# Performance work log

Hardware: AMD Instinct MI355X
Metric: run time of the kernel (lower is better)

The kernel has to match this reference:

```python
import jax, jax.numpy as jnp
import numpy as np

N_NODES = 50000
N_EDGES = 1600000
IN_CH = 128
HIDDEN = 64
OUT_DIM = 64
N_GRAPHS = 64


def setup_inputs() -> dict:
    key = jax.random.key(0)
    ks = jax.random.split(key, 8)
    x = jax.random.normal(ks[0], (N_NODES, IN_CH), dtype=jnp.float32)
    W1 = jax.random.normal(ks[1], (IN_CH, HIDDEN), dtype=jnp.float32) * (1.0 / np.sqrt(IN_CH))
    b1 = jnp.zeros((HIDDEN,), dtype=jnp.float32)
    W2 = jax.random.normal(ks[2], (HIDDEN, HIDDEN), dtype=jnp.float32) * (1.0 / np.sqrt(HIDDEN))
    b2 = jnp.zeros((HIDDEN,), dtype=jnp.float32)
    Wp = jax.random.normal(ks[3], (HIDDEN, OUT_DIM), dtype=jnp.float32) * (1.0 / np.sqrt(HIDDEN))
    bp = jnp.zeros((OUT_DIM,), dtype=jnp.float32)
    edge_index = jax.random.randint(ks[4], (2, N_EDGES), 0, N_NODES, dtype=jnp.int32)
    batch = jnp.sort(jax.random.randint(ks[5], (N_NODES,), 0, N_GRAPHS, dtype=jnp.int32))
    return {"x": x, "W1": W1, "b1": b1, "W2": W2, "b2": b2,
            "Wp": Wp, "bp": bp, "edge_index": edge_index, "batch": batch}


def _gcn_norm(edge_index, num_nodes):
    # add self-loops, then symmetric normalization D^{-1/2} (A+I) D^{-1/2}
    loop = jnp.arange(num_nodes, dtype=edge_index.dtype)
    src = jnp.concatenate([edge_index[0], loop])
    dst = jnp.concatenate([edge_index[1], loop])
    deg = jax.ops.segment_sum(jnp.ones_like(dst, dtype=jnp.float32), dst,
                              num_segments=num_nodes)
    dinv = jnp.where(deg > 0, jax.lax.rsqrt(deg), 0.0)
    norm = dinv[src] * dinv[dst]  # [E+N]
    return src, dst, norm


def _gcn_conv(x, W, b, src, dst, norm, num_nodes):
    h = x @ W                                  # [N, F_out] transform first (F_out small)
    msg = h[src] * norm[:, None]               # gather + scale  [E+N, F_out]
    agg = jax.ops.segment_sum(msg, dst, num_segments=num_nodes)
    return agg + b


def reference(x, W1, b1, W2, b2, Wp, bp, edge_index, batch):
    n = x.shape[0]
    src, dst, norm = _gcn_norm(edge_index, n)
    h = jax.nn.relu(_gcn_conv(x, W1, b1, src, dst, norm, n))
    # dropout: eval mode (identity)
    h = jax.nn.relu(_gcn_conv(h, W2, b2, src, dst, norm, n))
    # global mean pool over graphs in batch
    gsum = jax.ops.segment_sum(h, batch, num_segments=N_GRAPHS)
    cnt = jax.ops.segment_sum(jnp.ones((n,), dtype=h.dtype), batch,
                              num_segments=N_GRAPHS)
    g = gsum / jnp.maximum(cnt, 1.0)[:, None]
    return g @ Wp + bp
```

## Files before the change

kernel.cpp:

```cpp
#include <hip/hip_runtime.h>

#define N_NODES  50000
#define N_EDGESC 1600000
#define N_GRAPHS 64
#define NBUCK    196
#define CHUNK    2048
#define NBLK     782

static __device__ __forceinline__ unsigned short f2bf(float f) {
  unsigned u = __float_as_uint(f);
  u += 0x7FFF + ((u >> 16) & 1);
  return (unsigned short)(u >> 16);
}
static __device__ __forceinline__ float bfLo(unsigned u) {
  return __uint_as_float(u << 16);
}
static __device__ __forceinline__ float bfHi(unsigned u) {
  return __uint_as_float(u & 0xFFFF0000u);
}

static __device__ __forceinline__ int lowerb(const int* a, int n, int v) {
  int lo = 0, hi = n;
  while (lo < hi) { int m = (lo + hi) >> 1; if (a[m] < v) lo = m + 1; else hi = m; }
  return lo;
}

__global__ __launch_bounds__(256) void k_hist(const int* __restrict__ dst,
                                              int* __restrict__ bcnt,
                                              float* __restrict__ gsum, int E) {
  __shared__ int hist[NBUCK];
  int t = threadIdx.x, blk = blockIdx.x;
  if (t < NBUCK) hist[t] = 0;
  if (blk == 0) {
    for (int i = t; i < N_GRAPHS * 64; i += 256) gsum[i] = 0.f;
  }
  __syncthreads();
  int e0 = blk * CHUNK;
#pragma unroll
  for (int i = 0; i < CHUNK; i += 256) {
    int e = e0 + i + t;
    if (e < E) atomicAdd(&hist[dst[e] >> 8], 1);
  }
  __syncthreads();
  if (t < NBUCK) bcnt[(size_t)t * NBLK + blk] = hist[t];
}

__global__ __launch_bounds__(256) void k_cscan(int* __restrict__ bcnt,
                                               int* __restrict__ btot) {
  __shared__ int sm[256];
  int b = blockIdx.x, t = threadIdx.x;
  int* p = bcnt + (size_t)b * NBLK;
  int carry = 0;
  for (int tile = 0; tile < (NBLK + 255) / 256; ++tile) {
    int idx = tile * 256 + t;
    int v = (idx < NBLK) ? p[idx] : 0;
    sm[t] = v;
    __syncthreads();
    for (int o = 1; o < 256; o <<= 1) {
      int add = (t >= o) ? sm[t - o] : 0;
      __syncthreads();
      sm[t] += add;
      __syncthreads();
    }
    int incl = sm[t];
    int total = sm[255];
    if (idx < NBLK) p[idx] = incl - v + carry;
    carry += total;
    __syncthreads();
  }
  if (t == 0) btot[b] = carry;
}

__global__ __launch_bounds__(256) void k_scatter(const int* __restrict__ src,
                                                 const int* __restrict__ dst,
                                                 const int* __restrict__ bcnt,
                                                 const int* __restrict__ btot,
                                                 unsigned* __restrict__ bbuf, int E) {
  __shared__ int base[NBUCK], cur[NBUCK], sm[256];
  int t = threadIdx.x, blk = blockIdx.x;
  int v = (t < NBUCK) ? btot[t] : 0;
  sm[t] = v;
  __syncthreads();
  for (int o = 1; o < 256; o <<= 1) {
    int add = (t >= o) ? sm[t - o] : 0;
    __syncthreads();
    sm[t] += add;
    __syncthreads();
  }
  if (t < NBUCK) {
    base[t] = (sm[t] - v) + bcnt[(size_t)t * NBLK + blk];
    cur[t] = 0;
  }
  __syncthreads();
  int e0 = blk * CHUNK;
#pragma unroll
  for (int i = 0; i < CHUNK; i += 256) {
    int e = e0 + i + t;
    if (e < E) {
      int d = dst[e], b = d >> 8;
      int pos = base[b] + atomicAdd(&cur[b], 1);
      bbuf[pos] = ((unsigned)(d & 255) << 24) | (unsigned)src[e];
    }
  }
}

__global__ __launch_bounds__(512) void k_bsort(const unsigned* __restrict__ bbuf,
                                               const int* __restrict__ btot,
                                               int* __restrict__ csr,
                                               int* __restrict__ row_off,
                                               float* __restrict__ dinv) {
  __shared__ int hist[256], off[256], cur[256], sm[256];
  int b = blockIdx.x, t = threadIdx.x;
  if (t < 256) {
    int v = (t < NBUCK) ? btot[t] : 0;
    sm[t] = v;
    hist[t] = 0; cur[t] = 0;
  }
  __syncthreads();
  for (int o = 1; o < 256; o <<= 1) {
    int add = 0;
    if (t < 256 && t >= o) add = sm[t - o];
    __syncthreads();
    if (t < 256) sm[t] += add;
    __syncthreads();
  }
  int gb = (b > 0) ? sm[b - 1] : 0;
  int cnt = btot[b];
  const unsigned* bp = bbuf + gb;
  for (int i = t; i < cnt; i += 512) atomicAdd(&hist[bp[i] >> 24], 1);
  __syncthreads();
  if (t < 256) off[t] = hist[t];
  __syncthreads();
  for (int o = 1; o < 256; o <<= 1) {
    int add = 0;
    if (t < 256 && t >= o) add = off[t - o];
    __syncthreads();
    if (t < 256) off[t] += add;
    __syncthreads();
  }
  if (t < 256) {
    int excl = off[t] - hist[t];
    off[t] = excl;
    int idx = (b << 8) + t;
    if (idx <= N_NODES) row_off[idx] = gb + excl;
    if (idx < N_NODES)  dinv[idx] = rsqrtf((float)(hist[t] + 1));
  }
  __syncthreads();
  for (int i = t; i < cnt; i += 512) {
    unsigned v = bp[i];
    int ld = v >> 24;
    int pos = atomicAdd(&cur[ld], 1);
    csr[gb + off[ld] + pos] = (int)(v & 0xFFFFFFu);
  }
}

template <int K>
__global__ __launch_bounds__(256) void k_gemm(const float* __restrict__ x,
                                              const float* __restrict__ W,
                                              const float* __restrict__ dinv,
                                              unsigned short* __restrict__ out, int N) {
  constexpr int KS = 64;
  constexpr int KP = KS + 4;
  __shared__ float xs[64 * KP];
  __shared__ float Wl[KS * 64];
  const int t = threadIdx.x;
  const int lane = t & 63;
  const int w = t >> 6;
  const int n0 = blockIdx.x * 64;

  float acc[16];
#pragma unroll
  for (int j = 0; j < 16; ++j) acc[j] = 0.f;

  for (int h = 0; h < K / KS; ++h) {
#pragma unroll
    for (int i = 0; i < KS * 16 / 256; ++i) {
      int li = i * 256 + t;
      float4 v = reinterpret_cast<const float4*>(W + h * KS * 64)[li];
      *reinterpret_cast<float4*>(Wl + li * 4) = v;
    }
#pragma unroll
    for (int i = 0; i < 64 * (KS / 4) / 256; ++i) {
      int li = i * 256 + t;
      int row = li / (KS / 4), c4 = li % (KS / 4);
      int node = n0 + row;
      float4 v = make_float4(0.f, 0.f, 0.f, 0.f);
      if (node < N) v = reinterpret_cast<const float4*>(x + (size_t)node * K + h * KS)[c4];
      *reinterpret_cast<float4*>(xs + row * KP + c4 * 4) = v;
    }
    __syncthreads();

    const float* xr = xs + lane * KP;
    const float* wq = Wl + w * 16;
#pragma unroll 4
    for (int kp = 0; kp < KS / 4; ++kp) {
      float4 xv = *reinterpret_cast<const float4*>(xr + kp * 4);
#pragma unroll
      for (int q = 0; q < 4; ++q) {
        int k = kp * 4 + q;
        float xq = (q == 0) ? xv.x : (q == 1) ? xv.y : (q == 2) ? xv.z : xv.w;
        const float* wk = wq + k * 64;
        float4 w0 = *reinterpret_cast<const float4*>(wk);
        float4 w1 = *reinterpret_cast<const float4*>(wk + 4);
        float4 w2 = *reinterpret_cast<const float4*>(wk + 8);
        float4 w3 = *reinterpret_cast<const float4*>(wk + 12);
        acc[ 0] = fmaf(xq, w0.x, acc[ 0]);
        acc[ 1] = fmaf(xq, w0.y, acc[ 1]);
        acc[ 2] = fmaf(xq, w0.z, acc[ 2]);
        acc[ 3] = fmaf(xq, w0.w, acc[ 3]);
        acc[ 4] = fmaf(xq, w1.x, acc[ 4]);
        acc[ 5] = fmaf(xq, w1.y, acc[ 5]);
        acc[ 6] = fmaf(xq, w1.z, acc[ 6]);
        acc[ 7] = fmaf(xq, w1.w, acc[ 7]);
        acc[ 8] = fmaf(xq, w2.x, acc[ 8]);
        acc[ 9] = fmaf(xq, w2.y, acc[ 9]);
        acc[10] = fmaf(xq, w2.z, acc[10]);
        acc[11] = fmaf(xq, w2.w, acc[11]);
        acc[12] = fmaf(xq, w3.x, acc[12]);
        acc[13] = fmaf(xq, w3.y, acc[13]);
        acc[14] = fmaf(xq, w3.z, acc[14]);
        acc[15] = fmaf(xq, w3.w, acc[15]);
      }
    }
    __syncthreads();
  }

  int node = n0 + lane;
  if (node < N) {
    float dv = dinv[node];
    unsigned pk[8];
#pragma unroll
    for (int j = 0; j < 8; ++j) {
      unsigned lo = f2bf(acc[2 * j] * dv);
      unsigned hi = f2bf(acc[2 * j + 1] * dv);
      pk[j] = lo | (hi << 16);
    }
    unsigned* op = reinterpret_cast<unsigned*>(out + (size_t)node * 64 + w * 16);
    *reinterpret_cast<uint4*>(op)     = make_uint4(pk[0], pk[1], pk[2], pk[3]);
    *reinterpret_cast<uint4*>(op + 4) = make_uint4(pk[4], pk[5], pk[6], pk[7]);
  }
}

__global__ __launch_bounds__(256) void k_gather(const unsigned short* __restrict__ hs,
                                                const int* __restrict__ row_off,
                                                const int* __restrict__ csr,
                                                const float* __restrict__ dinv,
                                                const float* __restrict__ bias,
                                                float* __restrict__ out, int N) {
  const int lane = threadIdx.x & 63;
  const int slot = lane >> 3;
  const int pos  = lane & 7;
  int wid = blockIdx.x * 4 + (threadIdx.x >> 6);
  int stride = gridDim.x * 4;
  const uint4* hsq = reinterpret_cast<const uint4*>(hs);
  float4 bA = reinterpret_cast<const float4*>(bias)[pos * 2];
  float4 bB = reinterpret_cast<const float4*>(bias)[pos * 2 + 1];
  for (int i = wid; i < N; i += stride) {
    float a[8];
    {
      uint4 sv = hsq[(((unsigned)i) << 3) + pos];
      if (slot == 0) {
        a[0] = bfLo(sv.x); a[1] = bfHi(sv.x); a[2] = bfLo(sv.y); a[3] = bfHi(sv.y);
        a[4] = bfLo(sv.z); a[5] = bfHi(sv.z); a[6] = bfLo(sv.w); a[7] = bfHi(sv.w);
      } else {
#pragma unroll
        for (int k = 0; k < 8; ++k) a[k] = 0.f;
      }
    }
    const int s0 = row_off[i], s1 = row_off[i + 1];
    int j = s0;
    for (; j + 32 <= s1; j += 32) {
      int idx[4];
#pragma unroll
      for (int q = 0; q < 4; ++q) idx[q] = csr[j + 8 * q + slot];
      uint4 v[4];
#pragma unroll
      for (int q = 0; q < 4; ++q)
        v[q] = hsq[(((unsigned)idx[q]) << 3) + pos];
#pragma unroll
      for (int q = 0; q < 4; ++q) {
        a[0] += bfLo(v[q].x); a[1] += bfHi(v[q].x);
        a[2] += bfLo(v[q].y); a[3] += bfHi(v[q].y);
        a[4] += bfLo(v[q].z); a[5] += bfHi(v[q].z);
        a[6] += bfLo(v[q].w); a[7] += bfHi(v[q].w);
      }
    }
    if (j < s1) {
      int idx[4];
      bool ok[4];
#pragma unroll
      for (int q = 0; q < 4; ++q) {
        int e = j + 8 * q + slot;
        ok[q] = e < s1;
        idx[q] = csr[min(e, s1 - 1)];
      }
      uint4 v[4];
#pragma unroll
      for (int q = 0; q < 4; ++q)
        v[q] = hsq[(((unsigned)idx[q]) << 3) + pos];
#pragma unroll
      for (int q = 0; q < 4; ++q) {
        if (ok[q]) {
          a[0] += bfLo(v[q].x); a[1] += bfHi(v[q].x);
          a[2] += bfLo(v[q].y); a[3] += bfHi(v[q].y);
          a[4] += bfLo(v[q].z); a[5] += bfHi(v[q].z);
          a[6] += bfLo(v[q].w); a[7] += bfHi(v[q].w);
        }
      }
    }
#pragma unroll
    for (int k = 0; k < 8; ++k) {
      a[k] += __shfl_xor(a[k], 8);
      a[k] += __shfl_xor(a[k], 16);
      a[k] += __shfl_xor(a[k], 32);
    }
    if (slot == 0) {
      float dv = dinv[i];
      float4 rA, rB;
      rA.x = fmaxf(fmaf(a[0], dv, bA.x), 0.f);
      rA.y = fmaxf(fmaf(a[1], dv, bA.y), 0.f);
      rA.z = fmaxf(fmaf(a[2], dv, bA.z), 0.f);
      rA.w = fmaxf(fmaf(a[3], dv, bA.w), 0.f);
      rB.x = fmaxf(fmaf(a[4], dv, bB.x), 0.f);
      rB.y = fmaxf(fmaf(a[5], dv, bB.y), 0.f);
      rB.z = fmaxf(fmaf(a[6], dv, bB.z), 0.f);
      rB.w = fmaxf(fmaf(a[7], dv, bB.w), 0.f);
      float4* op = reinterpret_cast<float4*>(out + (((size_t)i) << 6) + pos * 8);
      op[0] = rA;
      op[1] = rB;
    }
  }
}

__global__ __launch_bounds__(256) void k_pool1(const float* __restrict__ h,
                                               const int* __restrict__ batch,
                                               float* __restrict__ gsum, int N) {
  int c = threadIdx.x & 63;
  int w = threadIdx.x >> 6;
  int r0 = blockIdx.x * 64 + w * 16;
  if (r0 >= N) return;
  int r1 = min(r0 + 16, N);
  int gprev = batch[r0];
  float acc = 0.f;
  for (int r = r0; r < r1; ++r) {
    int g = batch[r];
    if (g != gprev) { atomicAdd(&gsum[gprev * 64 + c], acc); acc = 0.f; gprev = g; }
    acc += h[(size_t)r * 64 + c];
  }
  atomicAdd(&gsum[gprev * 64 + c], acc);
}

__global__ void k_final(const float* __restrict__ gsum, const int* __restrict__ batch,
                        const float* __restrict__ Wp, const float* __restrict__ bp,
                        float* __restrict__ out, int N) {
  __shared__ int lb[5];
  int t = threadIdx.x;
  int g0 = blockIdx.x * 4;
  if (t < 5) lb[t] = lowerb(batch, N, g0 + t);
  __syncthreads();
  int idx = blockIdx.x * 256 + t;
  int g = idx >> 6, o = idx & 63, gl = g & 3;
  float cinv = 1.0f / fmaxf((float)(lb[gl + 1] - lb[gl]), 1.0f);
  float acc = 0.f;
#pragma unroll
  for (int k = 0; k < 64; ++k) acc += gsum[g * 64 + k] * Wp[k * 64 + o];
  out[idx] = fmaf(acc, cinv, bp[o]);
}

extern "C" void kernel_launch(void* const* d_in, const int* in_sizes, int n_in,
                              void* d_out, int out_size, void* d_ws, size_t ws_size,
                              hipStream_t stream) {
  const float* x    = (const float*)d_in[0];
  const float* W1   = (const float*)d_in[1];
  const float* b1   = (const float*)d_in[2];
  const float* W2   = (const float*)d_in[3];
  const float* b2   = (const float*)d_in[4];
  const float* Wp   = (const float*)d_in[5];
  const float* bp   = (const float*)d_in[6];
  const int*   ei   = (const int*)d_in[7];
  const int*   batch= (const int*)d_in[8];
  float* out = (float*)d_out;

  const int N = N_NODES, E = N_EDGESC;
  const int* src  = ei;
  const int* dstp = ei + E;

  char* wsb = (char*)d_ws;
  size_t o = 0;
  auto alloc = [&](size_t bytes) -> void* {
    void* p = wsb + o;
    o = (o + bytes + 255) & ~(size_t)255;
    return p;
  };
  int*      bcnt   = (int*)alloc((size_t)NBUCK * NBLK * 4);
  int*      btot   = (int*)alloc(NBUCK * 4);
  unsigned* bbuf   = (unsigned*)alloc((size_t)E * 4);
  int*      row_off= (int*)alloc((size_t)(N + 1) * 4);
  int*      csr    = (int*)alloc((size_t)E * 4);
  float*    dinv   = (float*)alloc((size_t)N * 4);
  unsigned short* bufBF = (unsigned short*)alloc((size_t)N * 64 * 2);
  float*    bufF   = (float*)alloc((size_t)N * 64 * 4);
  float*    gsum   = (float*)alloc(64 * 64 * 4);

  int gN64 = (N + 63) / 64;

  k_hist<<<NBLK, 256, 0, stream>>>(dstp, bcnt, gsum, E);
  k_cscan<<<NBUCK, 256, 0, stream>>>(bcnt, btot);
  k_scatter<<<NBLK, 256, 0, stream>>>(src, dstp, bcnt, btot, bbuf, E);
  k_bsort<<<NBUCK, 512, 0, stream>>>(bbuf, btot, csr, row_off, dinv);

  k_gemm<128><<<gN64, 256, 0, stream>>>(x, W1, dinv, bufBF, N);
  k_gather<<<2048, 256, 0, stream>>>(bufBF, row_off, csr, dinv, b1, bufF, N);
  k_gemm<64><<<gN64, 256, 0, stream>>>(bufF, W2, dinv, bufBF, N);
  k_gather<<<2048, 256, 0, stream>>>(bufBF, row_off, csr, dinv, b2, bufF, N);

  k_pool1<<<gN64, 256, 0, stream>>>(bufF, batch, gsum, N);
  k_final<<<16, 256, 0, stream>>>(gsum, batch, Wp, bp, out, N);
}
```

Baseline: 160.8 us.

## Fuse W2 transform into layer-1 gather and pooling into layer-2 gather

```diff
diff --git a/kernel.cpp b/kernel.cpp
--- a/kernel.cpp
+++ b/kernel.cpp
@@ -241,113 +241,203 @@
   }
 }
 
-__global__ __launch_bounds__(256) void k_gather(const unsigned short* __restrict__ hs,
-                                                const int* __restrict__ row_off,
-                                                const int* __restrict__ csr,
-                                                const float* __restrict__ dinv,
-                                                const float* __restrict__ bias,
-                                                float* __restrict__ out, int N) {
-  const int lane = threadIdx.x & 63;
-  const int slot = lane >> 3;
-  const int pos  = lane & 7;
-  int wid = blockIdx.x * 4 + (threadIdx.x >> 6);
-  int stride = gridDim.x * 4;
-  const uint4* hsq = reinterpret_cast<const uint4*>(hs);
-  float4 bA = reinterpret_cast<const float4*>(bias)[pos * 2];
-  float4 bB = reinterpret_cast<const float4*>(bias)[pos * 2 + 1];
-  for (int i = wid; i < N; i += stride) {
-    float a[8];
-    {
-      uint4 sv = hsq[(((unsigned)i) << 3) + pos];
-      if (slot == 0) {
-        a[0] = bfLo(sv.x); a[1] = bfHi(sv.x); a[2] = bfLo(sv.y); a[3] = bfHi(sv.y);
-        a[4] = bfLo(sv.z); a[5] = bfHi(sv.z); a[6] = bfLo(sv.w); a[7] = bfHi(sv.w);
-      } else {
-#pragma unroll
-        for (int k = 0; k < 8; ++k) a[k] = 0.f;
-      }
-    }
-    const int s0 = row_off[i], s1 = row_off[i + 1];
-    int j = s0;
-    for (; j + 32 <= s1; j += 32) {
-      int idx[4];
-#pragma unroll
-      for (int q = 0; q < 4; ++q) idx[q] = csr[j + 8 * q + slot];
-      uint4 v[4];
-#pragma unroll
-      for (int q = 0; q < 4; ++q)
-        v[q] = hsq[(((unsigned)idx[q]) << 3) + pos];
-#pragma unroll
-      for (int q = 0; q < 4; ++q) {
+static __device__ __forceinline__ void gather_row(const uint4* __restrict__ hsq,
+                                                  const int* __restrict__ csr,
+                                                  int i, int s0, int s1,
+                                                  int slot, int pos, float a[8]) {
+  {
+    uint4 sv = hsq[(((unsigned)i) << 3) + pos];
+    if (slot == 0) {
+      a[0] = bfLo(sv.x); a[1] = bfHi(sv.x); a[2] = bfLo(sv.y); a[3] = bfHi(sv.y);
+      a[4] = bfLo(sv.z); a[5] = bfHi(sv.z); a[6] = bfLo(sv.w); a[7] = bfHi(sv.w);
+    } else {
+#pragma unroll
+      for (int k = 0; k < 8; ++k) a[k] = 0.f;
+    }
+  }
+  int j = s0;
+  for (; j + 32 <= s1; j += 32) {
+    int idx[4];
+#pragma unroll
+    for (int q = 0; q < 4; ++q) idx[q] = csr[j + 8 * q + slot];
+    uint4 v[4];
+#pragma unroll
+    for (int q = 0; q < 4; ++q)
+      v[q] = hsq[(((unsigned)idx[q]) << 3) + pos];
+#pragma unroll
+    for (int q = 0; q < 4; ++q) {
+      a[0] += bfLo(v[q].x); a[1] += bfHi(v[q].x);
+      a[2] += bfLo(v[q].y); a[3] += bfHi(v[q].y);
+      a[4] += bfLo(v[q].z); a[5] += bfHi(v[q].z);
+      a[6] += bfLo(v[q].w); a[7] += bfHi(v[q].w);
+    }
+  }
+  if (j < s1) {
+    int idx[4];
+    bool ok[4];
+#pragma unroll
+    for (int q = 0; q < 4; ++q) {
+      int e = j + 8 * q + slot;
+      ok[q] = e < s1;
+      idx[q] = csr[min(e, s1 - 1)];
+    }
+    uint4 v[4];
+#pragma unroll
+    for (int q = 0; q < 4; ++q)
+      v[q] = hsq[(((unsigned)idx[q]) << 3) + pos];
+#pragma unroll
+    for (int q = 0; q < 4; ++q) {
+      if (ok[q]) {
         a[0] += bfLo(v[q].x); a[1] += bfHi(v[q].x);
         a[2] += bfLo(v[q].y); a[3] += bfHi(v[q].y);
         a[4] += bfLo(v[q].z); a[5] += bfHi(v[q].z);
         a[6] += bfLo(v[q].w); a[7] += bfHi(v[q].w);
       }
     }
-    if (j < s1) {
-      int idx[4];
-      bool ok[4];
+  }
+#pragma unroll
+  for (int k = 0; k < 8; ++k) {
+    a[k] += __shfl_xor(a[k], 8);
+    a[k] += __shfl_xor(a[k], 16);
+    a[k] += __shfl_xor(a[k], 32);
+  }
+}
+
+__global__ __launch_bounds__(256) void k_gather_w2(const unsigned short* __restrict__ hs,
+                                                   const int* __restrict__ row_off,
+                                                   const int* __restrict__ csr,
+                                                   const float* __restrict__ dinv,
+                                                   const float* __restrict__ b1,
+                                                   const float* __restrict__ W2,
+                                                   unsigned short* __restrict__ out2,
+                                                   int N) {
+  __shared__ float w2l[64 * 65];
+  const int t = threadIdx.x;
+  const int lane = t & 63;
+  const int slot = lane >> 3;
+  const int pos  = lane & 7;
+  if (t < 64) {
+#pragma unroll
+    for (int m = 0; m < 8; ++m) {
+      const float* gp = W2 + (pos * 8 + m) * 64 + slot * 8;
+      float4 wA = *reinterpret_cast<const float4*>(gp);
+      float4 wB = *reinterpret_cast<const float4*>(gp + 4);
+      float* dp = w2l + lane * 65 + m * 8;
+      *reinterpret_cast<float4*>(dp) = wA;
+      *reinterpret_cast<float4*>(dp + 4) = wB;
+    }
+  }
+  __syncthreads();
+
+  int wid = blockIdx.x * 4 + (t >> 6);
+  int stride = gridDim.x * 4;
+  const uint4* hsq = reinterpret_cast<const uint4*>(hs);
+  float4 bA = reinterpret_cast<const float4*>(b1)[pos * 2];
+  float4 bB = reinterpret_cast<const float4*>(b1)[pos * 2 + 1];
+  const float* wl = w2l + lane * 65;
+
+  for (int i = wid; i < N; i += stride) {
+    float a[8];
+    gather_row(hsq, csr, i, row_off[i], row_off[i + 1], slot, pos, a);
+    float dv = dinv[i];
+    float h1[8];
+    h1[0] = fmaxf(fmaf(a[0], dv, bA.x), 0.f);
+    h1[1] = fmaxf(fmaf(a[1], dv, bA.y), 0.f);
+    h1[2] = fmaxf(fmaf(a[2], dv, bA.z), 0.f);
+    h1[3] = fmaxf(fmaf(a[3], dv, bA.w), 0.f);
+    h1[4] = fmaxf(fmaf(a[4], dv, bB.x), 0.f);
+    h1[5] = fmaxf(fmaf(a[5], dv, bB.y), 0.f);
+    h1[6] = fmaxf(fmaf(a[6], dv, bB.z), 0.f);
+    h1[7] = fmaxf(fmaf(a[7], dv, bB.w), 0.f);
+    float p[8];
+#pragma unroll
+    for (int j = 0; j < 8; ++j) p[j] = 0.f;
+#pragma unroll
+    for (int m = 0; m < 8; ++m) {
+      float4 wA = *reinterpret_cast<const float4*>(wl + m * 8);
+      float4 wB = *reinterpret_cast<const float4*>(wl + m * 8 + 4);
+      p[0] = fmaf(h1[m], wA.x, p[0]);
+      p[1] = fmaf(h1[m], wA.y, p[1]);
+      p[2] = fmaf(h1[m], wA.z, p[2]);
+      p[3] = fmaf(h1[m], wA.w, p[3]);
+      p[4] = fmaf(h1[m], wB.x, p[4]);
+      p[5] = fmaf(h1[m], wB.y, p[5]);
+      p[6] = fmaf(h1[m], wB.z, p[6]);
+      p[7] = fmaf(h1[m], wB.w, p[7]);
+    }
+#pragma unroll
+    for (int j = 0; j < 8; ++j) {
+      p[j] += __shfl_xor(p[j], 1);
+      p[j] += __shfl_xor(p[j], 2);
+      p[j] += __shfl_xor(p[j], 4);
+    }
+    if (pos == 0) {
+      unsigned pk[4];
 #pragma unroll
       for (int q = 0; q < 4; ++q) {
-        int e = j + 8 * q + slot;
-        ok[q] = e < s1;
-        idx[q] = csr[min(e, s1 - 1)];
+        unsigned lo = f2bf(p[2 * q] * dv);
+        unsigned hi = f2bf(p[2 * q + 1] * dv);
+        pk[q] = lo | (hi << 16);
       }
-      uint4 v[4];
-#pragma unroll
-      for (int q = 0; q < 4; ++q)
-        v[q] = hsq[(((unsigned)idx[q]) << 3) + pos];
-#pragma unroll
-      for (int q = 0; q < 4; ++q) {
-        if (ok[q]) {
-          a[0] += bfLo(v[q].x); a[1] += bfHi(v[q].x);
-          a[2] += bfLo(v[q].y); a[3] += bfHi(v[q].y);
-          a[4] += bfLo(v[q].z); a[5] += bfHi(v[q].z);
-          a[6] += bfLo(v[q].w); a[7] += bfHi(v[q].w);
-        }
+      *reinterpret_cast<uint4*>(out2 + (((size_t)i) << 6) + slot * 8) =
+          make_uint4(pk[0], pk[1], pk[2], pk[3]);
+    }
+  }
+}
+
+__global__ __launch_bounds__(256) void k_gather_pool(const unsigned short* __restrict__ hs,
+                                                     const int* __restrict__ row_off,
+                                                     const int* __restrict__ csr,
+                                                     const float* __restrict__ dinv,
+                                                     const float* __restrict__ b2,
+                                                     const int* __restrict__ batch,
+                                                     float* __restrict__ gsum, int N) {
+  const int t = threadIdx.x;
+  const int lane = t & 63;
+  const int slot = lane >> 3;
+  const int pos  = lane & 7;
+  const int NPW = 4;
+  int base = (blockIdx.x * 4 + (t >> 6)) * NPW;
+  if (base >= N) return;
+  int end = min(base + NPW, N);
+  const uint4* hsq = reinterpret_cast<const uint4*>(hs);
+  float4 bA = reinterpret_cast<const float4*>(b2)[pos * 2];
+  float4 bB = reinterpret_cast<const float4*>(b2)[pos * 2 + 1];
+
+  float gacc[8];
+#pragma unroll
+  for (int j = 0; j < 8; ++j) gacc[j] = 0.f;
+  int gprev = batch[base];
+
+  for (int i = base; i < end; ++i) {
+    float a[8];
+    gather_row(hsq, csr, i, row_off[i], row_off[i + 1], slot, pos, a);
+    float dv = dinv[i];
+    int g = batch[i];
+    if (g != gprev) {
+      if (slot == 0) {
+#pragma unroll
+        for (int j = 0; j < 8; ++j)
+          atomicAdd(&gsum[gprev * 64 + pos * 8 + j], gacc[j]);
       }
-    }
-#pragma unroll
-    for (int k = 0; k < 8; ++k) {
-      a[k] += __shfl_xor(a[k], 8);
-      a[k] += __shfl_xor(a[k], 16);
-      a[k] += __shfl_xor(a[k], 32);
-    }
-    if (slot == 0) {
-      float dv = dinv[i];
-      float4 rA, rB;
-      rA.x = fmaxf(fmaf(a[0], dv, bA.x), 0.f);
-      rA.y = fmaxf(fmaf(a[1], dv, bA.y), 0.f);
-      rA.z = fmaxf(fmaf(a[2], dv, bA.z), 0.f);
-      rA.w = fmaxf(fmaf(a[3], dv, bA.w), 0.f);
-      rB.x = fmaxf(fmaf(a[4], dv, bB.x), 0.f);
-      rB.y = fmaxf(fmaf(a[5], dv, bB.y), 0.f);
-      rB.z = fmaxf(fmaf(a[6], dv, bB.z), 0.f);
-      rB.w = fmaxf(fmaf(a[7], dv, bB.w), 0.f);
-      float4* op = reinterpret_cast<float4*>(out + (((size_t)i) << 6) + pos * 8);
-      op[0] = rA;
-      op[1] = rB;
-    }
-  }
-}
-
-__global__ __launch_bounds__(256) void k_pool1(const float* __restrict__ h,
-                                               const int* __restrict__ batch,
-                                               float* __restrict__ gsum, int N) {
-  int c = threadIdx.x & 63;
-  int w = threadIdx.x >> 6;
-  int r0 = blockIdx.x * 64 + w * 16;
-  if (r0 >= N) return;
-  int r1 = min(r0 + 16, N);
-  int gprev = batch[r0];
-  float acc = 0.f;
-  for (int r = r0; r < r1; ++r) {
-    int g = batch[r];
-    if (g != gprev) { atomicAdd(&gsum[gprev * 64 + c], acc); acc = 0.f; gprev = g; }
-    acc += h[(size_t)r * 64 + c];
-  }
-  atomicAdd(&gsum[gprev * 64 + c], acc);
+#pragma unroll
+      for (int j = 0; j < 8; ++j) gacc[j] = 0.f;
+      gprev = g;
+    }
+    gacc[0] += fmaxf(fmaf(a[0], dv, bA.x), 0.f);
+    gacc[1] += fmaxf(fmaf(a[1], dv, bA.y), 0.f);
+    gacc[2] += fmaxf(fmaf(a[2], dv, bA.z), 0.f);
+    gacc[3] += fmaxf(fmaf(a[3], dv, bA.w), 0.f);
+    gacc[4] += fmaxf(fmaf(a[4], dv, bB.x), 0.f);
+    gacc[5] += fmaxf(fmaf(a[5], dv, bB.y), 0.f);
+    gacc[6] += fmaxf(fmaf(a[6], dv, bB.z), 0.f);
+    gacc[7] += fmaxf(fmaf(a[7], dv, bB.w), 0.f);
+  }
+  if (slot == 0) {
+#pragma unroll
+    for (int j = 0; j < 8; ++j)
+      atomicAdd(&gsum[gprev * 64 + pos * 8 + j], gacc[j]);
+  }
 }
 
 __global__ void k_final(const float* __restrict__ gsum, const int* __restrict__ batch,
@@ -398,22 +488,20 @@
   int*      row_off= (int*)alloc((size_t)(N + 1) * 4);
   int*      csr    = (int*)alloc((size_t)E * 4);
   float*    dinv   = (float*)alloc((size_t)N * 4);
-  unsigned short* bufBF = (unsigned short*)alloc((size_t)N * 64 * 2);
-  float*    bufF   = (float*)alloc((size_t)N * 64 * 4);
+  unsigned short* bufA = (unsigned short*)alloc((size_t)N * 64 * 2);
+  unsigned short* bufB = (unsigned short*)alloc((size_t)N * 64 * 2);
   float*    gsum   = (float*)alloc(64 * 64 * 4);
 
   int gN64 = (N + 63) / 64;
+  int gPool = (N + 15) / 16;
 
   k_hist<<<NBLK, 256, 0, stream>>>(dstp, bcnt, gsum, E);
   k_cscan<<<NBUCK, 256, 0, stream>>>(bcnt, btot);
   k_scatter<<<NBLK, 256, 0, stream>>>(src, dstp, bcnt, btot, bbuf, E);
   k_bsort<<<NBUCK, 512, 0, stream>>>(bbuf, btot, csr, row_off, dinv);
 
-  k_gemm<128><<<gN64, 256, 0, stream>>>(x, W1, dinv, bufBF, N);
-  k_gather<<<2048, 256, 0, stream>>>(bufBF, row_off, csr, dinv, b1, bufF, N);
-  k_gemm<64><<<gN64, 256, 0, stream>>>(bufF, W2, dinv, bufBF, N);
-  k_gather<<<2048, 256, 0, stream>>>(bufBF, row_off, csr, dinv, b2, bufF, N);
-
-  k_pool1<<<gN64, 256, 0, stream>>>(bufF, batch, gsum, N);
+  k_gemm<128><<<gN64, 256, 0, stream>>>(x, W1, dinv, bufA, N);
+  k_gather_w2<<<2048, 256, 0, stream>>>(bufA, row_off, csr, dinv, b1, W2, bufB, N);
+  k_gather_pool<<<gPool, 256, 0, stream>>>(bufB, row_off, csr, dinv, b2, batch, gsum, N);
   k_final<<<16, 256, 0, stream>>>(gsum, batch, Wp, bp, out, N);
 }
```

Result: slower. 264.9 us (+64.7%).

## Map eight nodes per wavefront in gather instead of one node per wave

Applied to the files above, without the earlier changes.

```diff
diff --git a/kernel.cpp b/kernel.cpp
--- a/kernel.cpp
+++ b/kernel.cpp
@@ -250,86 +250,60 @@
   const int lane = threadIdx.x & 63;
   const int slot = lane >> 3;
   const int pos  = lane & 7;
-  int wid = blockIdx.x * 4 + (threadIdx.x >> 6);
-  int stride = gridDim.x * 4;
+  int n0 = (blockIdx.x * 4 + (threadIdx.x >> 6)) * 8;
+  if (n0 >= N) return;
+  const int node = n0 + slot;
   const uint4* hsq = reinterpret_cast<const uint4*>(hs);
   float4 bA = reinterpret_cast<const float4*>(bias)[pos * 2];
   float4 bB = reinterpret_cast<const float4*>(bias)[pos * 2 + 1];
-  for (int i = wid; i < N; i += stride) {
-    float a[8];
-    {
-      uint4 sv = hsq[(((unsigned)i) << 3) + pos];
-      if (slot == 0) {
-        a[0] = bfLo(sv.x); a[1] = bfHi(sv.x); a[2] = bfLo(sv.y); a[3] = bfHi(sv.y);
-        a[4] = bfLo(sv.z); a[5] = bfHi(sv.z); a[6] = bfLo(sv.w); a[7] = bfHi(sv.w);
-      } else {
-#pragma unroll
-        for (int k = 0; k < 8; ++k) a[k] = 0.f;
-      }
-    }
-    const int s0 = row_off[i], s1 = row_off[i + 1];
-    int j = s0;
-    for (; j + 32 <= s1; j += 32) {
-      int idx[4];
-#pragma unroll
-      for (int q = 0; q < 4; ++q) idx[q] = csr[j + 8 * q + slot];
-      uint4 v[4];
-#pragma unroll
-      for (int q = 0; q < 4; ++q)
-        v[q] = hsq[(((unsigned)idx[q]) << 3) + pos];
-#pragma unroll
-      for (int q = 0; q < 4; ++q) {
+
+  const int s0 = row_off[node];
+  const int deg = row_off[node + 1] - s0;
+
+  float a[8];
+  {
+    uint4 sv = hsq[(((unsigned)node) << 3) + pos];
+    a[0] = bfLo(sv.x); a[1] = bfHi(sv.x); a[2] = bfLo(sv.y); a[3] = bfHi(sv.y);
+    a[4] = bfLo(sv.z); a[5] = bfHi(sv.z); a[6] = bfLo(sv.w); a[7] = bfHi(sv.w);
+  }
+
+  for (int e = 0; __any(e < deg); e += 4) {
+    int id[4];
+    bool ok[4];
+#pragma unroll
+    for (int q = 0; q < 4; ++q) {
+      int ei = e + q;
+      ok[q] = ei < deg;
+      id[q] = csr[s0 + max(min(ei, deg - 1), 0)];
+    }
+    uint4 v[4];
+#pragma unroll
+    for (int q = 0; q < 4; ++q)
+      v[q] = hsq[(((unsigned)id[q]) << 3) + pos];
+#pragma unroll
+    for (int q = 0; q < 4; ++q) {
+      if (ok[q]) {
         a[0] += bfLo(v[q].x); a[1] += bfHi(v[q].x);
         a[2] += bfLo(v[q].y); a[3] += bfHi(v[q].y);
         a[4] += bfLo(v[q].z); a[5] += bfHi(v[q].z);
         a[6] += bfLo(v[q].w); a[7] += bfHi(v[q].w);
       }
     }
-    if (j < s1) {
-      int idx[4];
-      bool ok[4];
-#pragma unroll
-      for (int q = 0; q < 4; ++q) {
-        int e = j + 8 * q + slot;
-        ok[q] = e < s1;
-        idx[q] = csr[min(e, s1 - 1)];
-      }
-      uint4 v[4];
-#pragma unroll
-      for (int q = 0; q < 4; ++q)
-        v[q] = hsq[(((unsigned)idx[q]) << 3) + pos];
-#pragma unroll
-      for (int q = 0; q < 4; ++q) {
-        if (ok[q]) {
-          a[0] += bfLo(v[q].x); a[1] += bfHi(v[q].x);
-          a[2] += bfLo(v[q].y); a[3] += bfHi(v[q].y);
-          a[4] += bfLo(v[q].z); a[5] += bfHi(v[q].z);
-          a[6] += bfLo(v[q].w); a[7] += bfHi(v[q].w);
-        }
-      }
-    }
-#pragma unroll
-    for (int k = 0; k < 8; ++k) {
-      a[k] += __shfl_xor(a[k], 8);
-      a[k] += __shfl_xor(a[k], 16);
-      a[k] += __shfl_xor(a[k], 32);
-    }
-    if (slot == 0) {
-      float dv = dinv[i];
-      float4 rA, rB;
-      rA.x = fmaxf(fmaf(a[0], dv, bA.x), 0.f);
-      rA.y = fmaxf(fmaf(a[1], dv, bA.y), 0.f);
-      rA.z = fmaxf(fmaf(a[2], dv, bA.z), 0.f);
-      rA.w = fmaxf(fmaf(a[3], dv, bA.w), 0.f);
-      rB.x = fmaxf(fmaf(a[4], dv, bB.x), 0.f);
-      rB.y = fmaxf(fmaf(a[5], dv, bB.y), 0.f);
-      rB.z = fmaxf(fmaf(a[6], dv, bB.z), 0.f);
-      rB.w = fmaxf(fmaf(a[7], dv, bB.w), 0.f);
-      float4* op = reinterpret_cast<float4*>(out + (((size_t)i) << 6) + pos * 8);
-      op[0] = rA;
-      op[1] = rB;
-    }
-  }
+  }
+
+  float dv = dinv[node];
+  float4 rA, rB;
+  rA.x = fmaxf(fmaf(a[0], dv, bA.x), 0.f);
+  rA.y = fmaxf(fmaf(a[1], dv, bA.y), 0.f);
+  rA.z = fmaxf(fmaf(a[2], dv, bA.z), 0.f);
+  rA.w = fmaxf(fmaf(a[3], dv, bA.w), 0.f);
+  rB.x = fmaxf(fmaf(a[4], dv, bB.x), 0.f);
+  rB.y = fmaxf(fmaf(a[5], dv, bB.y), 0.f);
+  rB.z = fmaxf(fmaf(a[6], dv, bB.z), 0.f);
+  rB.w = fmaxf(fmaf(a[7], dv, bB.w), 0.f);
+  float4* op = reinterpret_cast<float4*>(out + (((size_t)node) << 6) + pos * 8);
+  op[0] = rA;
+  op[1] = rB;
 }
 
 __global__ __launch_bounds__(256) void k_pool1(const float* __restrict__ h,
@@ -403,6 +377,7 @@
   float*    gsum   = (float*)alloc(64 * 64 * 4);
 
   int gN64 = (N + 63) / 64;
+  int gG   = (N + 31) / 32;
 
   k_hist<<<NBLK, 256, 0, stream>>>(dstp, bcnt, gsum, E);
   k_cscan<<<NBUCK, 256, 0, stream>>>(bcnt, btot);
@@ -410,9 +385,9 @@
   k_bsort<<<NBUCK, 512, 0, stream>>>(bbuf, btot, csr, row_off, dinv);
 
   k_gemm<128><<<gN64, 256, 0, stream>>>(x, W1, dinv, bufBF, N);
-  k_gather<<<2048, 256, 0, stream>>>(bufBF, row_off, csr, dinv, b1, bufF, N);
+  k_gather<<<gG, 256, 0, stream>>>(bufBF, row_off, csr, dinv, b1, bufF, N);
   k_gemm<64><<<gN64, 256, 0, stream>>>(bufF, W2, dinv, bufBF, N);
-  k_gather<<<2048, 256, 0, stream>>>(bufBF, row_off, csr, dinv, b2, bufF, N);
+  k_gather<<<gG, 256, 0, stream>>>(bufBF, row_off, csr, dinv, b2, bufF, N);
 
   k_pool1<<<gN64, 256, 0, stream>>>(bufF, batch, gsum, N);
   k_final<<<16, 256, 0, stream>>>(gsum, batch, Wp, bp, out, N);
```

Result: no change. 161.3 us (+0.3%).
